# Performance work log

Hardware: AMD Instinct MI355X
Metric: run time of the kernel (lower is better)

The kernel has to match this reference:

```python
import jax, jax.numpy as jnp
import numpy as np

N = 50000   # nodes per sample
H = 5000    # hyperedges
E = 400000  # incidence entries
B = 2       # batch
C = 64      # channels (in == out, heads = 1)
NEG_SLOPE = 0.2


def setup_inputs() -> dict:
    key = jax.random.key(0)
    k1, k2, k3, k4, k5 = jax.random.split(key, 5)
    x = jax.random.normal(k1, (B, N, C), jnp.float32)
    # glorot-ish scales for params
    weight = jax.random.normal(k2, (C, C), jnp.float32) * (1.0 / np.sqrt(C))
    att = jax.random.normal(k3, (1, 1, 2 * C), jnp.float32) * 0.1
    node_idx = jax.random.randint(k4, (E,), 0, N)
    # sorted so hyperedge ids appear in order (matches dict insertion order in source)
    hedge_idx = jnp.sort(jax.random.randint(k5, (E,), 0, H))
    return {"x": x, "weight": weight, "att": att,
            "node_idx": node_idx, "hedge_idx": hedge_idx}


def reference(x, weight, att, node_idx, hedge_idx):
    # x: [B,N,C] -> project and move node dim first: x1 [N,B,C]
    xw = jnp.einsum('bnc,cd->bnd', x, weight)
    x1 = jnp.transpose(xw, (1, 0, 2))

    xi = x1[node_idx]  # gather per incidence: [E,B,C]
    # per-hyperedge sum of member node features (the dict loop in source)
    edge_sums = jax.ops.segment_sum(xi, hedge_idx, num_segments=H)  # [H,B,C]
    xj = edge_sums[hedge_idx]  # [E,B,C]

    # attention logits: ([E,B,2C] * att[1,1,2C]).sum(-1) -> [E,B]
    alpha = (jnp.concatenate([xi, xj], axis=-1) * att).sum(-1)
    alpha = jnp.where(alpha >= 0, alpha, NEG_SLOPE * alpha)  # leaky_relu

    # segment softmax over node ids (num_nodes = N), stable
    seg_max = jax.ops.segment_max(alpha, node_idx, num_segments=N)
    seg_max = jnp.where(jnp.isfinite(seg_max), seg_max, 0.0)
    ex = jnp.exp(alpha - seg_max[node_idx])
    denom = jax.ops.segment_sum(ex, node_idx, num_segments=N)
    alpha = ex / denom[node_idx]  # [E,B]; dropout is identity in eval

    ones = jnp.ones((node_idx.shape[0],), x.dtype)
    Dn = jax.ops.segment_sum(ones, node_idx, num_segments=N)   # node degree (NOT inverted in source)
    De = jax.ops.segment_sum(ones, hedge_idx, num_segments=H)
    Binv = jnp.where(De > 0, 1.0 / De, 0.0)                    # 1/deg, inf -> 0

    # pass 1 (source_to_target): nodes -> hyperedges, norm = Binv[edge]
    m = jax.ops.segment_sum(Binv[hedge_idx][:, None, None] * alpha[:, :, None] * xi,
                            hedge_idx, num_segments=H)          # [H,B,C]
    # pass 2 (target_to_source): hyperedges -> nodes, norm = Dn[node]
    out = jax.ops.segment_sum(Dn[node_idx][:, None, None] * alpha[:, :, None] * m[hedge_idx],
                              node_idx, num_segments=N)         # [N,B,C]
    return jnp.transpose(out, (1, 0, 2))  # [B,N,C]
```

## Files before the change

### kernel.cpp

```cpp
#include <hip/hip_runtime.h>
#include <math.h>

#define N_NODES 50000
#define N_HEDGE 5000
#define N_EDGES 400000
#define NB 2
#define NC 64
#define NEG 0.2f
#define NROWS (N_NODES * NB)

#define ALLOC_BLOCKS ((N_NODES + 255) / 256)
#define HEDGE_BLOCKS ((N_HEDGE + 3) / 4)

__device__ __forceinline__ unsigned short f2bf(float f) {
    unsigned int u = __float_as_uint(f);
    unsigned int r = (u + 0x7FFFu + ((u >> 16) & 1u)) >> 16;
    return (unsigned short)r;
}

__device__ __forceinline__ float lrelu_exp(float r) {
    r = (r >= 0.f) ? r : NEG * r;
    r = fmaxf(r, -80.f);
    return __expf(r);
}

__global__ __launch_bounds__(256, 4) void gemm_kernel(const float* __restrict__ x,
                                                      const float* __restrict__ W,
                                                      const float* __restrict__ att,
                                                      const int* __restrict__ node_idx,
                                                      const int* __restrict__ hedge_idx,
                                                      unsigned short* __restrict__ xwb,
                                                      float* __restrict__ p1,
                                                      float* __restrict__ p2,
                                                      int* __restrict__ cnt,
                                                      int* __restrict__ rank,
                                                      int* __restrict__ estart)
{
    __shared__ float xs[64 * 68];
    __shared__ float Ws[64 * 68];
    int t = threadIdx.x;
    int R = blockIdx.x * 64;

    int gid = blockIdx.x * 256 + t;
    if (gid < N_EDGES) {
        rank[gid] = atomicAdd(&cnt[node_idx[gid]], 1);
    }
    if (gid <= N_HEDGE) {
        int lo = 0, hi = N_EDGES;
        while (lo < hi) {
            int mid = (lo + hi) >> 1;
            if (hedge_idx[mid] < gid) lo = mid + 1; else hi = mid;
        }
        estart[gid] = lo;
    }

#pragma unroll
    for (int i = 0; i < 4; i++) {
        int lin = t + 256 * i;
        int r = lin >> 4, c4 = lin & 15;
        float4 wv = ((const float4*)W)[lin];
        *(float4*)&Ws[r * 68 + c4 * 4] = wv;
        int g = R + r;
        float4 xv = make_float4(0.f, 0.f, 0.f, 0.f);
        if (g < NROWS) {
            int n = g >> 1, b = g & 1;
            xv = ((const float4*)(x + ((size_t)b * N_NODES + n) * NC))[c4];
        }
        *(float4*)&xs[r * 68 + c4 * 4] = xv;
    }
    __syncthreads();

    int tr = t >> 4, tc = t & 15;
    float acc[4][4];
#pragma unroll
    for (int i = 0; i < 4; i++)
#pragma unroll
        for (int j = 0; j < 4; j++) acc[i][j] = 0.f;

#pragma unroll 4
    for (int k4 = 0; k4 < 16; k4++) {
        float4 xv[4], wv[4];
#pragma unroll
        for (int i = 0; i < 4; i++)
            xv[i] = *(const float4*)&xs[(tr * 4 + i) * 68 + k4 * 4];
#pragma unroll
        for (int kk = 0; kk < 4; kk++)
            wv[kk] = *(const float4*)&Ws[(k4 * 4 + kk) * 68 + tc * 4];
#pragma unroll
        for (int i = 0; i < 4; i++) {
            acc[i][0] = fmaf(xv[i].x, wv[0].x, acc[i][0]);
            acc[i][1] = fmaf(xv[i].x, wv[0].y, acc[i][1]);
            acc[i][2] = fmaf(xv[i].x, wv[0].z, acc[i][2]);
            acc[i][3] = fmaf(xv[i].x, wv[0].w, acc[i][3]);
            acc[i][0] = fmaf(xv[i].y, wv[1].x, acc[i][0]);
            acc[i][1] = fmaf(xv[i].y, wv[1].y, acc[i][1]);
            acc[i][2] = fmaf(xv[i].y, wv[1].z, acc[i][2]);
            acc[i][3] = fmaf(xv[i].y, wv[1].w, acc[i][3]);
            acc[i][0] = fmaf(xv[i].z, wv[2].x, acc[i][0]);
            acc[i][1] = fmaf(xv[i].z, wv[2].y, acc[i][1]);
            acc[i][2] = fmaf(xv[i].z, wv[2].z, acc[i][2]);
            acc[i][3] = fmaf(xv[i].z, wv[2].w, acc[i][3]);
            acc[i][0] = fmaf(xv[i].w, wv[3].x, acc[i][0]);
            acc[i][1] = fmaf(xv[i].w, wv[3].y, acc[i][1]);
            acc[i][2] = fmaf(xv[i].w, wv[3].z, acc[i][2]);
            acc[i][3] = fmaf(xv[i].w, wv[3].w, acc[i][3]);
        }
    }

    float a1x = att[tc * 4], a1y = att[tc * 4 + 1], a1z = att[tc * 4 + 2], a1w = att[tc * 4 + 3];
    float a2x = att[64 + tc * 4], a2y = att[64 + tc * 4 + 1], a2z = att[64 + tc * 4 + 2], a2w = att[64 + tc * 4 + 3];
#pragma unroll
    for (int i = 0; i < 4; i++) {
        int g = R + tr * 4 + i;
        if (g < NROWS) {
            ushort4 bv;
            bv.x = f2bf(acc[i][0]); bv.y = f2bf(acc[i][1]);
            bv.z = f2bf(acc[i][2]); bv.w = f2bf(acc[i][3]);
            ((ushort4*)(xwb + (size_t)g * 64))[tc] = bv;
        }
        float v1 = acc[i][0] * a1x + acc[i][1] * a1y + acc[i][2] * a1z + acc[i][3] * a1w;
        float v2 = acc[i][0] * a2x + acc[i][1] * a2y + acc[i][2] * a2z + acc[i][3] * a2w;
#pragma unroll
        for (int off = 8; off >= 1; off >>= 1) {
            v1 += __shfl_xor(v1, off, 64);
            v2 += __shfl_xor(v2, off, 64);
        }
        if (tc == 0 && g < NROWS) { p1[g] = v1; p2[g] = v2; }
    }
}

__global__ __launch_bounds__(256) void ah_kernel(const int* __restrict__ cnt,
                                                 int* __restrict__ base,
                                                 int* __restrict__ gcursor,
                                                 const float* __restrict__ p2,
                                                 const int* __restrict__ node_idx,
                                                 const int* __restrict__ estart,
                                                 float* __restrict__ s2)
{
    if (blockIdx.x < ALLOC_BLOCKS) {
        __shared__ int sm[256];
        __shared__ int bbase;
        int tid = threadIdx.x;
        int i = blockIdx.x * 256 + tid;
        int v = (i < N_NODES) ? cnt[i] : 0;
        sm[tid] = v;
        __syncthreads();
        for (int off = 1; off < 256; off <<= 1) {
            int t2 = (tid >= off) ? sm[tid - off] : 0;
            __syncthreads();
            sm[tid] += t2;
            __syncthreads();
        }
        if (tid == 255) bbase = atomicAdd(gcursor, sm[255]);
        __syncthreads();
        if (i < N_NODES) base[i] = bbase + sm[tid] - v;
    } else {
        int wv = (blockIdx.x - ALLOC_BLOCKS) * 4 + (threadIdx.x >> 6);
        if (wv >= N_HEDGE) return;
        int lane = threadIdx.x & 63;
        int s = estart[wv], e1 = estart[wv + 1];
        float a0 = 0.f, a1 = 0.f;
        for (int e = s + lane; e < e1; e += 64) {
            int n = node_idx[e];
            float2 p = ((const float2*)p2)[n];
            a0 += p.x; a1 += p.y;
        }
#pragma unroll
        for (int off = 32; off >= 1; off >>= 1) {
            a0 += __shfl_xor(a0, off, 64);
            a1 += __shfl_xor(a1, off, 64);
        }
        if (lane == 0) { s2[wv * 2] = a0; s2[wv * 2 + 1] = a1; }
    }
}

__global__ __launch_bounds__(256) void scatter_kernel(const int* __restrict__ node_idx,
                                                      const int* __restrict__ hedge_idx,
                                                      const int* __restrict__ rank,
                                                      const int* __restrict__ base,
                                                      int* __restrict__ hperm)
{
    int e = blockIdx.x * 256 + threadIdx.x;
    if (e >= N_EDGES) return;
    int n = node_idx[e];
    hperm[base[n] + rank[e]] = hedge_idx[e];
}

__global__ __launch_bounds__(256) void den_kernel(const int* __restrict__ base,
                                                  const int* __restrict__ cnt,
                                                  const int* __restrict__ hperm,
                                                  const float* __restrict__ p1,
                                                  const float* __restrict__ s2,
                                                  float* __restrict__ den)
{
    int t = threadIdx.x;
    int n = blockIdx.x * 32 + (t >> 3);
    if (n >= N_NODES) return;
    int sub = t & 7;
    int s = base[n];
    int e1 = s + cnt[n];
    float2 pn = ((const float2*)p1)[n];
    const float2* s2v = (const float2*)s2;
    float a0 = 0.f, a1 = 0.f;
    for (int j = s + sub; j < e1; j += 8) {
        float2 v = s2v[hperm[j]];
        a0 += lrelu_exp(pn.x + v.x);
        a1 += lrelu_exp(pn.y + v.y);
    }
#pragma unroll
    for (int off = 1; off < 8; off <<= 1) {
        a0 += __shfl_xor(a0, off, 64);
        a1 += __shfl_xor(a1, off, 64);
    }
    if (sub == 0) ((float2*)den)[n] = make_float2(a0, a1);
}

__global__ __launch_bounds__(256) void m_kernel(const unsigned short* __restrict__ xwb,
                                                const int* __restrict__ node_idx,
                                                const int* __restrict__ estart,
                                                const float* __restrict__ p1,
                                                const float* __restrict__ s2,
                                                const float* __restrict__ den,
                                                float* __restrict__ m)
{
    __shared__ float red[3][128];
    int h = blockIdx.x;
    int t = threadIdx.x;
    int w = t >> 6, l = t & 63;
    int g = l >> 4;
    int i = l & 15;
    int b = i >> 3;
    int s = estart[h], e1 = estart[h + 1];
    float2 s2h = ((const float2*)s2)[h];
    float sb = b ? s2h.y : s2h.x;

    float c0 = 0.f, c1 = 0.f, c2 = 0.f, c3 = 0.f;
    float c4 = 0.f, c5 = 0.f, c6 = 0.f, c7 = 0.f;

    for (int eb = s + 4 * w; eb < e1; eb += 32) {
        int eA = eb + g;
        bool vA = eA < e1;
        int nA = node_idx[vA ? eA : s];
        float pA = p1[2 * nA + b];
        float dA = den[2 * nA + b];
        uint4 qA = *(const uint4*)&xwb[(size_t)nA * 128 + 8 * i];
        int eB = eb + 16 + g;
        bool vB = eB < e1;
        int nB = node_idx[vB ? eB : s];
        float pB = p1[2 * nB + b];
        float dB = den[2 * nB + b];
        uint4 qB = *(const uint4*)&xwb[(size_t)nB * 128 + 8 * i];

        float aA = lrelu_exp(pA + sb) * __builtin_amdgcn_rcpf(dA);
        aA = vA ? aA : 0.f;
        float aB = lrelu_exp(pB + sb) * __builtin_amdgcn_rcpf(dB);
        aB = vB ? aB : 0.f;

        c0 = fmaf(aA, __uint_as_float(qA.x << 16), c0);
        c1 = fmaf(aA, __uint_as_float(qA.x & 0xffff0000u), c1);
        c2 = fmaf(aA, __uint_as_float(qA.y << 16), c2);
        c3 = fmaf(aA, __uint_as_float(qA.y & 0xffff0000u), c3);
        c4 = fmaf(aA, __uint_as_float(qA.z << 16), c4);
        c5 = fmaf(aA, __uint_as_float(qA.z & 0xffff0000u), c5);
        c6 = fmaf(aA, __uint_as_float(qA.w << 16), c6);
        c7 = fmaf(aA, __uint_as_float(qA.w & 0xffff0000u), c7);
        c0 = fmaf(aB, __uint_as_float(qB.x << 16), c0);
        c1 = fmaf(aB, __uint_as_float(qB.x & 0xffff0000u), c1);
        c2 = fmaf(aB, __uint_as_float(qB.y << 16), c2);
        c3 = fmaf(aB, __uint_as_float(qB.y & 0xffff0000u), c3);
        c4 = fmaf(aB, __uint_as_float(qB.z << 16), c4);
        c5 = fmaf(aB, __uint_as_float(qB.z & 0xffff0000u), c5);
        c6 = fmaf(aB, __uint_as_float(qB.w << 16), c6);
        c7 = fmaf(aB, __uint_as_float(qB.w & 0xffff0000u), c7);
    }

#pragma unroll
    for (int off = 16; off <= 32; off <<= 1) {
        c0 += __shfl_xor(c0, off, 64);
        c1 += __shfl_xor(c1, off, 64);
        c2 += __shfl_xor(c2, off, 64);
        c3 += __shfl_xor(c3, off, 64);
        c4 += __shfl_xor(c4, off, 64);
        c5 += __shfl_xor(c5, off, 64);
        c6 += __shfl_xor(c6, off, 64);
        c7 += __shfl_xor(c7, off, 64);
    }
    if (w && l < 16) {
        float* r = &red[w - 1][8 * l];
        r[0] = c0; r[1] = c1; r[2] = c2; r[3] = c3;
        r[4] = c4; r[5] = c5; r[6] = c6; r[7] = c7;
    }
    __syncthreads();
    if (w == 0 && l < 16) {
#pragma unroll
        for (int k = 0; k < 3; k++) {
            const float* r = &red[k][8 * l];
            c0 += r[0]; c1 += r[1]; c2 += r[2]; c3 += r[3];
            c4 += r[4]; c5 += r[5]; c6 += r[6]; c7 += r[7];
        }
        int d = e1 - s;
        float binv = (d > 0) ? 1.0f / (float)d : 0.0f;
        float* dst = m + (size_t)h * 128 + 8 * l;
        *(float4*)dst = make_float4(binv * c0, binv * c1, binv * c2, binv * c3);
        *(float4*)(dst + 4) = make_float4(binv * c4, binv * c5, binv * c6, binv * c7);
    }
}

__global__ __launch_bounds__(256) void out_kernel(const float* __restrict__ m,
                                                  const int* __restrict__ hperm,
                                                  const float* __restrict__ p1,
                                                  const float* __restrict__ s2,
                                                  const int* __restrict__ base,
                                                  const int* __restrict__ cnt,
                                                  const float* __restrict__ den,
                                                  float* __restrict__ out)
{
    int n = blockIdx.x * 4 + (threadIdx.x >> 6);
    if (n >= N_NODES) return;
    int l = threadIdx.x & 63;
    int g = l >> 5;
    int i = l & 31;
    int b = i >> 4;
    int d = cnt[n];
    int s = base[n];
    int e1 = s + d;
    float pnb = p1[2 * n + b];
    const float2* s2v = (const float2*)s2;
    float c0 = 0.f, c1 = 0.f, c2 = 0.f, c3 = 0.f;

    for (int jb = s; jb < e1; jb += 8) {
        int jA = jb + g;     bool vA = jA < e1;
        int jB = jb + 2 + g; bool vB = jB < e1;
        int jC = jb + 4 + g; bool vC = jC < e1;
        int jD = jb + 6 + g; bool vD = jD < e1;
        int hA = hperm[vA ? jA : s];
        int hB = hperm[vB ? jB : s];
        int hC = hperm[vC ? jC : s];
        int hD = hperm[vD ? jD : s];
        float2 wA = s2v[hA], wB = s2v[hB], wC = s2v[hC], wD = s2v[hD];
        float4 mA = *(const float4*)(m + (size_t)hA * 128 + 4 * i);
        float4 mB = *(const float4*)(m + (size_t)hB * 128 + 4 * i);
        float4 mC = *(const float4*)(m + (size_t)hC * 128 + 4 * i);
        float4 mD = *(const float4*)(m + (size_t)hD * 128 + 4 * i);
        float aA = lrelu_exp(pnb + (b ? wA.y : wA.x)); aA = vA ? aA : 0.f;
        float aB = lrelu_exp(pnb + (b ? wB.y : wB.x)); aB = vB ? aB : 0.f;
        float aC = lrelu_exp(pnb + (b ? wC.y : wC.x)); aC = vC ? aC : 0.f;
        float aD = lrelu_exp(pnb + (b ? wD.y : wD.x)); aD = vD ? aD : 0.f;
        c0 = fmaf(aA, mA.x, c0); c1 = fmaf(aA, mA.y, c1);
        c2 = fmaf(aA, mA.z, c2); c3 = fmaf(aA, mA.w, c3);
        c0 = fmaf(aB, mB.x, c0); c1 = fmaf(aB, mB.y, c1);
        c2 = fmaf(aB, mB.z, c2); c3 = fmaf(aB, mB.w, c3);
        c0 = fmaf(aC, mC.x, c0); c1 = fmaf(aC, mC.y, c1);
        c2 = fmaf(aC, mC.z, c2); c3 = fmaf(aC, mC.w, c3);
        c0 = fmaf(aD, mD.x, c0); c1 = fmaf(aD, mD.y, c1);
        c2 = fmaf(aD, mD.z, c2); c3 = fmaf(aD, mD.w, c3);
    }
    c0 += __shfl_xor(c0, 32, 64);
    c1 += __shfl_xor(c1, 32, 64);
    c2 += __shfl_xor(c2, 32, 64);
    c3 += __shfl_xor(c3, 32, 64);
    if (l < 32) {
        float dd = den[2 * n + b];
        float scale = (d > 0) ? (float)d * __builtin_amdgcn_rcpf(dd) : 0.f;
        int c = (4 * i) & 63;
        float* dst = out + (size_t)b * N_NODES * 64 + (size_t)n * 64 + c;
        __builtin_nontemporal_store(scale * c0, &dst[0]);
        __builtin_nontemporal_store(scale * c1, &dst[1]);
        __builtin_nontemporal_store(scale * c2, &dst[2]);
        __builtin_nontemporal_store(scale * c3, &dst[3]);
    }
}

extern "C" void kernel_launch(void* const* d_in, const int* in_sizes, int n_in,
                              void* d_out, int out_size, void* d_ws, size_t ws_size,
                              hipStream_t stream)
{
    const float* x      = (const float*)d_in[0];
    const float* W      = (const float*)d_in[1];
    const float* att    = (const float*)d_in[2];
    const int* node_idx = (const int*)d_in[3];
    const int* hedge_idx= (const int*)d_in[4];
    float* out = (float*)d_out;

    unsigned short* xwb = (unsigned short*)d_ws;
    float* p1     = (float*)(xwb + (size_t)NROWS * NC);
    float* p2     = p1 + NROWS;
    float* s2     = p2 + NROWS;
    float* m      = s2 + 10000;
    float* den    = m + (size_t)N_HEDGE * NB * NC;
    int* estart  = (int*)(den + NROWS);
    int* cnt     = estart + 5008;
    int* gcursor = cnt + N_NODES;
    int* base    = gcursor + 8;
    int* hperm   = base + N_NODES;
    int* rank    = hperm + N_EDGES;

    hipMemsetAsync(cnt, 0, (size_t)(N_NODES + 8) * sizeof(int), stream);

    gemm_kernel<<<(NROWS + 63) / 64, 256, 0, stream>>>(x, W, att, node_idx, hedge_idx,
                                                       xwb, p1, p2, cnt, rank, estart);
    ah_kernel<<<ALLOC_BLOCKS + HEDGE_BLOCKS, 256, 0, stream>>>(cnt, base, gcursor,
                                                               p2, node_idx, estart, s2);
    scatter_kernel<<<(N_EDGES + 255) / 256, 256, 0, stream>>>(node_idx, hedge_idx,
                                                              rank, base, hperm);
    den_kernel<<<(N_NODES + 31) / 32, 256, 0, stream>>>(base, cnt, hperm, p1, s2, den);
    m_kernel<<<N_HEDGE, 256, 0, stream>>>(xwb, node_idx, estart, p1, s2, den, m);
    out_kernel<<<(N_NODES + 3) / 4, 256, 0, stream>>>(m, hperm, p1, s2, base, cnt, den, out);
}
```

Measured before the change: 172.0 us.

## Unroll gathers in m and hedge-sum kernels, recompute softmax denominator in out_kernel

Moves the atomic rank/count and binary-search code in the GEMM kernel to after the matrix math, so those memory ops no longer delay the tile loads. Unrolls the hyperedge p2 reduction by two and the m_kernel gather loop from two to four incidences per iteration, putting more independent loads in flight. out_kernel now sums its own exp terms as the softmax denominator instead of reading den, which drops a dependency and a load. The costs are more registers in m_kernel, and out_kernel's denominator is now summed in a different order than den_kernel's, so results may differ slightly in the last bits.

```diff
diff --git a/kernel.cpp b/kernel.cpp
--- a/kernel.cpp
+++ b/kernel.cpp
@@ -40,19 +40,6 @@
     __shared__ float Ws[64 * 68];
     int t = threadIdx.x;
     int R = blockIdx.x * 64;
-
-    int gid = blockIdx.x * 256 + t;
-    if (gid < N_EDGES) {
-        rank[gid] = atomicAdd(&cnt[node_idx[gid]], 1);
-    }
-    if (gid <= N_HEDGE) {
-        int lo = 0, hi = N_EDGES;
-        while (lo < hi) {
-            int mid = (lo + hi) >> 1;
-            if (hedge_idx[mid] < gid) lo = mid + 1; else hi = mid;
-        }
-        estart[gid] = lo;
-    }
 
 #pragma unroll
     for (int i = 0; i < 4; i++) {
@@ -127,6 +114,19 @@
         }
         if (tc == 0 && g < NROWS) { p1[g] = v1; p2[g] = v2; }
     }
+
+    int gid = blockIdx.x * 256 + t;
+    if (gid < N_EDGES) {
+        rank[gid] = atomicAdd(&cnt[node_idx[gid]], 1);
+    }
+    if (gid <= N_HEDGE) {
+        int lo = 0, hi = N_EDGES;
+        while (lo < hi) {
+            int mid = (lo + hi) >> 1;
+            if (hedge_idx[mid] < gid) lo = mid + 1; else hi = mid;
+        }
+        estart[gid] = lo;
+    }
 }
 
 __global__ __launch_bounds__(256) void ah_kernel(const int* __restrict__ cnt,
@@ -160,10 +160,14 @@
         int lane = threadIdx.x & 63;
         int s = estart[wv], e1 = estart[wv + 1];
         float a0 = 0.f, a1 = 0.f;
-        for (int e = s + lane; e < e1; e += 64) {
-            int n = node_idx[e];
-            float2 p = ((const float2*)p2)[n];
-            a0 += p.x; a1 += p.y;
+        for (int e = s + lane; e < e1; e += 128) {
+            int eB = e + 64; bool vB = eB < e1;
+            int nA = node_idx[e];
+            int nB = node_idx[vB ? eB : s];
+            float2 pA = ((const float2*)p2)[nA];
+            float2 pB = ((const float2*)p2)[nB];
+            a0 += pA.x + (vB ? pB.x : 0.f);
+            a1 += pA.y + (vB ? pB.y : 0.f);
         }
 #pragma unroll
         for (int off = 32; off >= 1; off >>= 1) {
@@ -237,24 +241,28 @@
     float c0 = 0.f, c1 = 0.f, c2 = 0.f, c3 = 0.f;
     float c4 = 0.f, c5 = 0.f, c6 = 0.f, c7 = 0.f;
 
-    for (int eb = s + 4 * w; eb < e1; eb += 32) {
-        int eA = eb + g;
-        bool vA = eA < e1;
+    for (int eb = s + 4 * w; eb < e1; eb += 64) {
+        int eA = eb + g;      bool vA = eA < e1;
+        int eB = eb + 16 + g; bool vB = eB < e1;
+        int eC = eb + 32 + g; bool vC = eC < e1;
+        int eD = eb + 48 + g; bool vD = eD < e1;
         int nA = node_idx[vA ? eA : s];
-        float pA = p1[2 * nA + b];
-        float dA = den[2 * nA + b];
+        int nB = node_idx[vB ? eB : s];
+        int nC = node_idx[vC ? eC : s];
+        int nD = node_idx[vD ? eD : s];
+        float pA = p1[2 * nA + b], pB = p1[2 * nB + b];
+        float pC = p1[2 * nC + b], pD = p1[2 * nD + b];
+        float dA = den[2 * nA + b], dB = den[2 * nB + b];
+        float dC = den[2 * nC + b], dD = den[2 * nD + b];
         uint4 qA = *(const uint4*)&xwb[(size_t)nA * 128 + 8 * i];
-        int eB = eb + 16 + g;
-        bool vB = eB < e1;
-        int nB = node_idx[vB ? eB : s];
-        float pB = p1[2 * nB + b];
-        float dB = den[2 * nB + b];
         uint4 qB = *(const uint4*)&xwb[(size_t)nB * 128 + 8 * i];
-
-        float aA = lrelu_exp(pA + sb) * __builtin_amdgcn_rcpf(dA);
-        aA = vA ? aA : 0.f;
-        float aB = lrelu_exp(pB + sb) * __builtin_amdgcn_rcpf(dB);
-        aB = vB ? aB : 0.f;
+        uint4 qC = *(const uint4*)&xwb[(size_t)nC * 128 + 8 * i];
+        uint4 qD = *(const uint4*)&xwb[(size_t)nD * 128 + 8 * i];
+
+        float aA = lrelu_exp(pA + sb) * __builtin_amdgcn_rcpf(dA); aA = vA ? aA : 0.f;
+        float aB = lrelu_exp(pB + sb) * __builtin_amdgcn_rcpf(dB); aB = vB ? aB : 0.f;
+        float aC = lrelu_exp(pC + sb) * __builtin_amdgcn_rcpf(dC); aC = vC ? aC : 0.f;
+        float aD = lrelu_exp(pD + sb) * __builtin_amdgcn_rcpf(dD); aD = vD ? aD : 0.f;
 
         c0 = fmaf(aA, __uint_as_float(qA.x << 16), c0);
         c1 = fmaf(aA, __uint_as_float(qA.x & 0xffff0000u), c1);
@@ -272,6 +280,22 @@
         c5 = fmaf(aB, __uint_as_float(qB.z & 0xffff0000u), c5);
         c6 = fmaf(aB, __uint_as_float(qB.w << 16), c6);
         c7 = fmaf(aB, __uint_as_float(qB.w & 0xffff0000u), c7);
+        c0 = fmaf(aC, __uint_as_float(qC.x << 16), c0);
+        c1 = fmaf(aC, __uint_as_float(qC.x & 0xffff0000u), c1);
+        c2 = fmaf(aC, __uint_as_float(qC.y << 16), c2);
+        c3 = fmaf(aC, __uint_as_float(qC.y & 0xffff0000u), c3);
+        c4 = fmaf(aC, __uint_as_float(qC.z << 16), c4);
+        c5 = fmaf(aC, __uint_as_float(qC.z & 0xffff0000u), c5);
+        c6 = fmaf(aC, __uint_as_float(qC.w << 16), c6);
+        c7 = fmaf(aC, __uint_as_float(qC.w & 0xffff0000u), c7);
+        c0 = fmaf(aD, __uint_as_float(qD.x << 16), c0);
+        c1 = fmaf(aD, __uint_as_float(qD.x & 0xffff0000u), c1);
+        c2 = fmaf(aD, __uint_as_float(qD.y << 16), c2);
+        c3 = fmaf(aD, __uint_as_float(qD.y & 0xffff0000u), c3);
+        c4 = fmaf(aD, __uint_as_float(qD.z << 16), c4);
+        c5 = fmaf(aD, __uint_as_float(qD.z & 0xffff0000u), c5);
+        c6 = fmaf(aD, __uint_as_float(qD.w << 16), c6);
+        c7 = fmaf(aD, __uint_as_float(qD.w & 0xffff0000u), c7);
     }
 
 #pragma unroll
@@ -312,7 +336,6 @@
                                                   const float* __restrict__ s2,
                                                   const int* __restrict__ base,
                                                   const int* __restrict__ cnt,
-                                                  const float* __restrict__ den,
                                                   float* __restrict__ out)
 {
     int n = blockIdx.x * 4 + (threadIdx.x >> 6);
@@ -326,7 +349,7 @@
     int e1 = s + d;
     float pnb = p1[2 * n + b];
     const float2* s2v = (const float2*)s2;
-    float c0 = 0.f, c1 = 0.f, c2 = 0.f, c3 = 0.f;
+    float c0 = 0.f, c1 = 0.f, c2 = 0.f, c3 = 0.f, sden = 0.f;
 
     for (int jb = s; jb < e1; jb += 8) {
         int jA = jb + g;     bool vA = jA < e1;
@@ -346,6 +369,7 @@
         float aB = lrelu_exp(pnb + (b ? wB.y : wB.x)); aB = vB ? aB : 0.f;
         float aC = lrelu_exp(pnb + (b ? wC.y : wC.x)); aC = vC ? aC : 0.f;
         float aD = lrelu_exp(pnb + (b ? wD.y : wD.x)); aD = vD ? aD : 0.f;
+        sden += ((aA + aB) + aC) + aD;
         c0 = fmaf(aA, mA.x, c0); c1 = fmaf(aA, mA.y, c1);
         c2 = fmaf(aA, mA.z, c2); c3 = fmaf(aA, mA.w, c3);
         c0 = fmaf(aB, mB.x, c0); c1 = fmaf(aB, mB.y, c1);
@@ -359,9 +383,9 @@
     c1 += __shfl_xor(c1, 32, 64);
     c2 += __shfl_xor(c2, 32, 64);
     c3 += __shfl_xor(c3, 32, 64);
+    sden += __shfl_xor(sden, 32, 64);
     if (l < 32) {
-        float dd = den[2 * n + b];
-        float scale = (d > 0) ? (float)d * __builtin_amdgcn_rcpf(dd) : 0.f;
+        float scale = (d > 0) ? (float)d * __builtin_amdgcn_rcpf(sden) : 0.f;
         int c = (4 * i) & 63;
         float* dst = out + (size_t)b * N_NODES * 64 + (size_t)n * 64 + c;
         __builtin_nontemporal_store(scale * c0, &dst[0]);
@@ -405,5 +429,5 @@
                                                               rank, base, hperm);
     den_kernel<<<(N_NODES + 31) / 32, 256, 0, stream>>>(base, cnt, hperm, p1, s2, den);
     m_kernel<<<N_HEDGE, 256, 0, stream>>>(xwb, node_idx, estart, p1, s2, den, m);
-    out_kernel<<<(N_NODES + 3) / 4, 256, 0, stream>>>(m, hperm, p1, s2, base, cnt, den, out);
-}
+    out_kernel<<<(N_NODES + 3) / 4, 256, 0, stream>>>(m, hperm, p1, s2, base, cnt, out);
+}
```

Result: faster. 165.2 us (-4.0%).
